# Kernel tuning notes

Measured on AMD Instinct MI355X. Metric: run time of the kernel, lower is better.

## Reference

```python
import jax, jax.numpy as jnp
import numpy as np

N_NODES = 50000
N_EDGES = 800000
IN_DIM = 128
HEADS = 4
CH = 64
NEG_SLOPE = 0.2


def _gat_conv(x, src, dst, W, a_src, a_dst, bias):
    """PyG-style GATConv (self-loops already appended to src/dst).
    x: [N, F_in], W: [F_in, H*C], a_src/a_dst: [H, C], bias: [H*C]."""
    n = x.shape[0]
    h = (x @ W).reshape(n, HEADS, CH)                      # [N, H, C]
    alpha_s = (h * a_src).sum(-1)                          # [N, H]
    alpha_d = (h * a_dst).sum(-1)                          # [N, H]
    e = jax.nn.leaky_relu(alpha_s[src] + alpha_d[dst], NEG_SLOPE)  # [E, H]
    m = jax.ops.segment_max(e, dst, num_segments=n)        # segment softmax over dst
    e = jnp.exp(e - m[dst])
    denom = jax.ops.segment_sum(e, dst, num_segments=n)
    alpha = e / (denom[dst] + 1e-16)                       # [E, H]
    out = jax.ops.segment_sum(h[src] * alpha[:, :, None], dst, num_segments=n)
    return out.reshape(n, HEADS * CH) + bias               # concat=True


def setup_inputs() -> dict:
    key = jax.random.key(0)
    ks = jax.random.split(key, 10)
    x = jax.random.normal(ks[0], (N_NODES, IN_DIM), dtype=jnp.float32)
    edge_index = jax.random.randint(ks[1], (2, N_EDGES), 0, N_NODES, dtype=jnp.int64)
    s1 = 1.0 / np.sqrt(IN_DIM)
    s2 = 1.0 / np.sqrt(HEADS * CH)
    return {
        "x": x,
        "edge_index": edge_index,
        "W1": jax.random.normal(ks[2], (IN_DIM, HEADS * CH), dtype=jnp.float32) * s1,
        "a_src1": jax.random.normal(ks[3], (HEADS, CH), dtype=jnp.float32) * s1,
        "a_dst1": jax.random.normal(ks[4], (HEADS, CH), dtype=jnp.float32) * s1,
        "b1": jnp.zeros((HEADS * CH,), dtype=jnp.float32),
        "W2": jax.random.normal(ks[5], (HEADS * CH, HEADS * CH), dtype=jnp.float32) * s2,
        "a_src2": jax.random.normal(ks[6], (HEADS, CH), dtype=jnp.float32) * s2,
        "a_dst2": jax.random.normal(ks[7], (HEADS, CH), dtype=jnp.float32) * s2,
        "b2": jnp.zeros((HEADS * CH,), dtype=jnp.float32),
        "fc_w": jax.random.normal(ks[8], (HEADS * CH, 1), dtype=jnp.float32) * s2,
        "fc_b": jnp.zeros((1,), dtype=jnp.float32),
    }


def reference(x, edge_index, W1, a_src1, a_dst1, b1, W2, a_src2, a_dst2, b2, fc_w, fc_b):
    n = x.shape[0]
    loop = jnp.arange(n, dtype=edge_index.dtype)           # PyG GATConv adds self-loops
    src = jnp.concatenate([edge_index[0], loop])
    dst = jnp.concatenate([edge_index[1], loop])
    h = jax.nn.elu(_gat_conv(x, src, dst, W1, a_src1, a_dst1, b1))
    h = jax.nn.elu(_gat_conv(h, src, dst, W2, a_src2, a_dst2, b2))
    return jax.nn.sigmoid(h @ fc_w + fc_b)                 # [N, 1]
```

## Files before the change

### kernel.cpp

```cpp
#include <hip/hip_runtime.h>
#include <hip/hip_bf16.h>

#define N_NODES 50000
#define N_EDGES 800000
#define NCHUNK 256
#define EPC 3125
#define NBUCKET 196
#define SCAN_N 50176
#define SCAN_BLOCKS 196

typedef __attribute__((ext_vector_type(8))) short bf16x8;
typedef __attribute__((ext_vector_type(4))) float f32x4;
typedef __attribute__((ext_vector_type(2))) float f32x2;
typedef unsigned short ushort_t;

__device__ __forceinline__ float bf2f(unsigned short u) {
    union { unsigned u32; float f; } v; v.u32 = (unsigned)u << 16; return v.f;
}
__device__ __forceinline__ unsigned short f2bf(float f) {
    __hip_bfloat16 h = __float2bfloat16(f);
    return *reinterpret_cast<unsigned short*>(&h);
}
__device__ __forceinline__ f32x2 bfpair(unsigned u) {
    union { unsigned a; float f; } lo, hi;
    lo.a = u << 16;
    hi.a = u & 0xFFFF0000u;
    f32x2 r; r.x = lo.f; r.y = hi.f; return r;
}
__device__ __forceinline__ void pkfma(f32x2& d, f32x2 a, f32x2 b) {
    asm("v_pk_fma_f32 %0, %1, %2, %0" : "+v"(d) : "v"(a), "v"(b));
}
__device__ __forceinline__ void gload16(const void* src, void* lds) {
    __builtin_amdgcn_global_load_lds(
        (const __attribute__((address_space(1))) unsigned int*)src,
        (__attribute__((address_space(3))) unsigned int*)lds, 16, 0, 0);
}

__device__ __forceinline__ int detect_is32_block(const unsigned* __restrict__ w,
                                                 int* s_is32, int tid) {
    if (tid == 0) {
        unsigned o = 0;
#pragma unroll
        for (int k = 1; k < 32; k += 2) o |= w[k];
        *s_is32 = (o != 0u);
    }
    __syncthreads();
    return *s_is32;
}

__device__ __forceinline__ int edge_elem(const unsigned* __restrict__ w, int is32, long long idx) {
    return is32 ? (int)w[idx] : (int)w[2 * idx];
}

#define CONV_BLOCKS 6250
#define PREP_W_BLOCKS (CONV_BLOCKS + 128 + 256)
__global__ void __launch_bounds__(256) prep_kernel(const float* __restrict__ x,
                                                   ushort_t* __restrict__ xbf,
                                                   const float* __restrict__ W1,
                                                   ushort_t* __restrict__ W1t,
                                                   const float* __restrict__ W2,
                                                   ushort_t* __restrict__ W2t,
                                                   const unsigned* __restrict__ ew,
                                                   int* __restrict__ chunkHist) {
    int b = blockIdx.x, t = threadIdx.x;
    if (b < CONV_BLOCKS) {
        int i = b * 256 + t;
        float4 v = ((const float4*)x)[i];
        ushort4 o;
        o.x = f2bf(v.x); o.y = f2bf(v.y); o.z = f2bf(v.z); o.w = f2bf(v.w);
        ((ushort4*)xbf)[i] = o;
    } else if (b < CONV_BLOCKS + 128) {
        int id = (b - CONV_BLOCKS) * 256 + t;
        int n = id >> 7, k = id & 127;
        W1t[id] = f2bf(W1[k * 256 + n]);
    } else if (b < CONV_BLOCKS + 128 + 256) {
        int id = (b - CONV_BLOCKS - 128) * 256 + t;
        int n = id >> 8, k = id & 255;
        W2t[id] = f2bf(W2[k * 256 + n]);
    } else {
        __shared__ int s_is32;
        __shared__ int hist[NBUCKET];
        int c = b - PREP_W_BLOCKS;
        int is32 = detect_is32_block(ew, &s_is32, t);
        for (int k = t; k < NBUCKET; k += 256) hist[k] = 0;
        __syncthreads();
        long long e0 = (long long)c * EPC;
        for (int k = t; k < EPC; k += 256) {
            int d = edge_elem(ew, is32, (long long)N_EDGES + e0 + k);
            atomicAdd(&hist[d >> 8], 1);
        }
        __syncthreads();
        for (int k = t; k < NBUCKET; k += 256)
            chunkHist[k * NCHUNK + c] = hist[k];
    }
}

__global__ void __launch_bounds__(256) scan1_kernel(const int* __restrict__ in,
                                                    int* __restrict__ excl, int* __restrict__ bsum) {
    __shared__ int s[256];
    int b = blockIdx.x, t = threadIdx.x, i = b * 256 + t;
    int v = in[i];
    s[t] = v;
    __syncthreads();
    for (int off = 1; off < 256; off <<= 1) {
        int y = (t >= off) ? s[t - off] : 0;
        __syncthreads();
        s[t] += y;
        __syncthreads();
    }
    excl[i] = s[t] - v;
    if (t == 255) bsum[b] = s[255];
}

__global__ void __launch_bounds__(256) scan2_kernel(const int* __restrict__ bsum,
                                                    int* __restrict__ boff) {
    __shared__ int s[256];
    int t = threadIdx.x;
    int v = (t < SCAN_BLOCKS) ? bsum[t] : 0;
    s[t] = v;
    __syncthreads();
    for (int off = 1; off < 256; off <<= 1) {
        int y = (t >= off) ? s[t - off] : 0;
        __syncthreads();
        s[t] += y;
        __syncthreads();
    }
    if (t < SCAN_BLOCKS) boff[t] = s[t] - v;
}

__global__ void __launch_bounds__(256) scan3_kernel(const int* __restrict__ boff,
                                                    int* __restrict__ excl) {
    int i = blockIdx.x * 256 + threadIdx.x;
    excl[i] += boff[blockIdx.x];
}

__global__ void __launch_bounds__(256) bucket_scatter_kernel(const unsigned* __restrict__ ew,
                                                             const int* __restrict__ chunkOff,
                                                             unsigned* __restrict__ ebuf) {
    __shared__ int s_is32;
    __shared__ int cur[NBUCKET];
    int t = threadIdx.x, b = blockIdx.x;
    int is32 = detect_is32_block(ew, &s_is32, t);
    for (int k = t; k < NBUCKET; k += 256) cur[k] = chunkOff[k * NCHUNK + b];
    __syncthreads();
    long long e0 = (long long)b * EPC;
    for (int k = t; k < EPC; k += 256) {
        long long e = e0 + k;
        unsigned s = (unsigned)edge_elem(ew, is32, e);
        int d = edge_elem(ew, is32, (long long)N_EDGES + e);
        int pos = atomicAdd(&cur[d >> 8], 1);
        ebuf[pos] = s | ((unsigned)d << 16);
    }
}

__global__ void __launch_bounds__(256) bucket_sort_kernel(const unsigned* __restrict__ ebuf,
                                                          const int* __restrict__ chunkOff,
                                                          unsigned* __restrict__ edge_csr,
                                                          int* __restrict__ row_ptr,
                                                          int* __restrict__ dhist) {
    __shared__ int cnt[256];
    __shared__ int s[256];
    __shared__ int dh[64];
    int b = blockIdx.x, t = threadIdx.x;
    int start = chunkOff[b * NCHUNK];
    int end = (b + 1 < NBUCKET) ? chunkOff[(b + 1) * NCHUNK] : N_EDGES;
    cnt[t] = 0;
    if (t < 64) dh[t] = 0;
    __syncthreads();
    for (int e = start + t; e < end; e += 256) {
        int d = (int)(ebuf[e] >> 16);
        atomicAdd(&cnt[d & 255], 1);
    }
    __syncthreads();
    int node = b * 256 + t;
    int mydeg = cnt[t];
    if (node < N_NODES) atomicAdd(&dh[mydeg < 63 ? mydeg : 63], 1);
    s[t] = mydeg;
    __syncthreads();
    for (int off = 1; off < 256; off <<= 1) {
        int y = (t >= off) ? s[t - off] : 0;
        __syncthreads();
        s[t] += y;
        __syncthreads();
    }
    int excl = s[t] - mydeg;
    if (node <= N_NODES) row_ptr[node] = start + excl;
    cnt[t] = start + excl;
    __syncthreads();
    for (int e = start + t; e < end; e += 256) {
        unsigned pk = ebuf[e];
        int pos = atomicAdd(&cnt[(pk >> 16) & 255], 1);
        edge_csr[pos] = pk;
    }
    if (t < 64 && dh[t]) atomicAdd(&dhist[t], dh[t]);
}

__global__ void __launch_bounds__(64) dscan_kernel(const int* __restrict__ dhist,
                                                   int* __restrict__ dcur) {
    int t = threadIdx.x;
    int v = dhist[t];
    int sum = v;
#pragma unroll
    for (int off = 1; off < 64; off <<= 1) {
        int y = __shfl_up(sum, off, 64);
        if (t >= off) sum += y;
    }
    dcur[t] = sum - v;
}

__global__ void __launch_bounds__(256) dscatter_kernel(const int* __restrict__ row_ptr,
                                                       int* __restrict__ dcur,
                                                       int* __restrict__ perm) {
    __shared__ int lh[64], lbase[64];
    int t = threadIdx.x, i = blockIdx.x * 256 + t;
    if (t < 64) lh[t] = 0;
    __syncthreads();
    int deg = 0;
    if (i < N_NODES) {
        deg = row_ptr[i + 1] - row_ptr[i];
        if (deg > 63) deg = 63;
        atomicAdd(&lh[deg], 1);
    }
    __syncthreads();
    if (t < 64) {
        lbase[t] = lh[t] ? atomicAdd(&dcur[t], lh[t]) : 0;
        lh[t] = 0;
    }
    __syncthreads();
    if (i < N_NODES) {
        int rank = atomicAdd(&lh[deg], 1);
        perm[lbase[deg] + rank] = i;
    }
}

template <int K>
__global__ void __launch_bounds__(256) mfma_gemm_kernel(const ushort_t* __restrict__ A,
                                                        const ushort_t* __restrict__ Wt,
                                                        void* __restrict__ Cv, int M,
                                                        const float* __restrict__ a_src,
                                                        const float* __restrict__ a_dst,
                                                        float* __restrict__ alpha_s,
                                                        float* __restrict__ alpha_d) {
    constexpr int CPR = K / 8;
    constexpr int NT = K / 64;
    __shared__ ushort_t Bs[64 * K];
    __shared__ ushort_t As[2][64 * 64];
    __shared__ float ps[64][2], pd[64][2];

    int tid = threadIdx.x;
    int wave = tid >> 6, lane = tid & 63;
    int l15 = lane & 15, l4 = lane >> 4;
    int wr = wave >> 1, wc = wave & 1;
    int colblock = blockIdx.x;
    int rowblock = blockIdx.y;

    for (int base = 0; base < 64 * CPR; base += 256) {
        int p = base + wave * 64 + lane;
        int row = p / CPR;
        int cs = p % CPR;
        int c = cs ^ (row & 7);
        const ushort_t* src = Wt + (long long)(colblock * 64 + row) * K + c * 8;
        void* dst = ((char*)Bs) + (base + wave * 64) * 16;
        gload16(src, dst);
    }
    {
        int r = lane >> 3, cs = lane & 7;
        int c = cs ^ r;
#pragma unroll
        for (int q = 0; q < 2; ++q) {
            int lrow = wave * 16 + q * 8;
            int grow = rowblock * 64 + lrow + r;
            if (grow >= M) grow = M - 1;
            const ushort_t* src = A + (long long)grow * K + c * 8;
            void* dst = ((char*)&As[0][0]) + lrow * 128;
            gload16(src, dst);
        }
    }
    __syncthreads();

    f32x4 acc[2][2] = {};
#pragma unroll
    for (int t = 0; t < NT; ++t) {
        if (t + 1 < NT) {
            int r = lane >> 3, cs = lane & 7;
            int c = cs ^ r;
#pragma unroll
            for (int q = 0; q < 2; ++q) {
                int lrow = wave * 16 + q * 8;
                int grow = rowblock * 64 + lrow + r;
                if (grow >= M) grow = M - 1;
                const ushort_t* src = A + (long long)grow * K + (t + 1) * 64 + c * 8;
                void* dst = ((char*)&As[(t + 1) & 1][0]) + lrow * 128;
                gload16(src, dst);
            }
        }
        const ushort_t* At = &As[t & 1][0];
#pragma unroll
        for (int w = 0; w < 2; ++w) {
            bf16x8 a[2], b[2];
#pragma unroll
            for (int mi = 0; mi < 2; ++mi) {
                int row = wr * 32 + mi * 16 + l15;
                int slot = (w * 4 + l4) ^ (l15 & 7);
                a[mi] = *(const bf16x8*)&At[row * 64 + slot * 8];
            }
#pragma unroll
            for (int ni = 0; ni < 2; ++ni) {
                int brow = wc * 32 + ni * 16 + l15;
                int slot = (t * 8 + w * 4 + l4) ^ (l15 & 7);
                b[ni] = *(const bf16x8*)&Bs[brow * CPR * 8 + slot * 8];
            }
#pragma unroll
            for (int mi = 0; mi < 2; ++mi)
#pragma unroll
                for (int ni = 0; ni < 2; ++ni)
                    acc[mi][ni] = __builtin_amdgcn_mfma_f32_16x16x32_bf16(a[mi], b[ni],
                                                                          acc[mi][ni], 0, 0, 0);
        }
        __syncthreads();
    }

    {
        float as0 = a_src[colblock * 64 + wc * 32 + l15];
        float as1 = a_src[colblock * 64 + wc * 32 + 16 + l15];
        float ad0 = a_dst[colblock * 64 + wc * 32 + l15];
        float ad1 = a_dst[colblock * 64 + wc * 32 + 16 + l15];
#pragma unroll
        for (int mi = 0; mi < 2; ++mi)
#pragma unroll
            for (int q = 0; q < 4; ++q) {
                float sv = acc[mi][0][q] * as0 + acc[mi][1][q] * as1;
                float dv = acc[mi][0][q] * ad0 + acc[mi][1][q] * ad1;
#pragma unroll
                for (int w = 1; w < 16; w <<= 1) {
                    sv += __shfl_xor(sv, w, 64);
                    dv += __shfl_xor(dv, w, 64);
                }
                if (l15 == 0) {
                    int row = wr * 32 + mi * 16 + l4 * 4 + q;
                    ps[row][wc] = sv;
                    pd[row][wc] = dv;
                }
            }
    }

    ushort_t* ep = ((ushort_t*)&As[0][0]) + wave * 1280;
#pragma unroll
    for (int mi = 0; mi < 2; ++mi)
#pragma unroll
        for (int ni = 0; ni < 2; ++ni)
#pragma unroll
            for (int q = 0; q < 4; ++q) {
                int row = mi * 16 + l4 * 4 + q;
                int col = ni * 16 + l15;
                ep[row * 40 + col] = f2bf(acc[mi][ni][q]);
            }
    __syncthreads();
#pragma unroll
    for (int j = 0; j < 2; ++j) {
        int p = lane * 2 + j;
        int row = p >> 2, seg = p & 3;
        uint4 v = *(const uint4*)&ep[row * 40 + seg * 8];
        int grow = rowblock * 64 + wr * 32 + row;
        int gcol = colblock * 64 + wc * 32 + seg * 8;
        if (grow < M) {
            f32x2 f01 = bfpair(v.x), f23 = bfpair(v.y);
            f32x2 f45 = bfpair(v.z), f67 = bfpair(v.w);
            int d0 = 0, d1 = 0;
            d0 = __builtin_amdgcn_cvt_pk_fp8_f32(f01.x, f01.y, d0, false);
            d0 = __builtin_amdgcn_cvt_pk_fp8_f32(f23.x, f23.y, d0, true);
            d1 = __builtin_amdgcn_cvt_pk_fp8_f32(f45.x, f45.y, d1, false);
            d1 = __builtin_amdgcn_cvt_pk_fp8_f32(f67.x, f67.y, d1, true);
            uint2 o; o.x = (unsigned)d0; o.y = (unsigned)d1;
            *(uint2*)((char*)Cv + (long long)grow * 256 + gcol) = o;
        }
    }
    if (tid < 64) {
        int ga = rowblock * 64 + tid;
        if (ga < M) {
            alpha_s[ga * 4 + colblock] = ps[tid][0] + ps[tid][1];
            alpha_d[ga * 4 + colblock] = pd[tid][0] + pd[tid][1];
        }
    }
}

template <int LAYER>
__global__ void __launch_bounds__(256) aggregate_kernel(
    const void* __restrict__ gv, const float* __restrict__ alpha_s,
    const float* __restrict__ alpha_d, const int* __restrict__ row_ptr,
    const unsigned* __restrict__ edge_csr, const int* __restrict__ perm,
    const float* __restrict__ bias, ushort_t* __restrict__ out_bf,
    const float* __restrict__ fc_w, const float* __restrict__ fc_b,
    float* __restrict__ final_out) {
    int wave = threadIdx.x >> 6;
    int lane = threadIdx.x & 63;
    int i = __builtin_amdgcn_readfirstlane(perm[blockIdx.x * 4 + wave]);
    int hd = lane >> 4;
    const char* gb = (const char*)gv;
    unsigned loff = (unsigned)(lane << 2);

    float ad = alpha_d[i * 4 + hd];
    float e0 = alpha_s[i * 4 + hd] + ad;
    e0 = e0 > 0.f ? e0 : 0.2f * e0;
    float w0 = __expf(e0);
    f32x2 wp0; wp0.x = w0; wp0.y = w0;
    f32x2 acc01 = {0.f, 0.f}, acc23 = {0.f, 0.f};
    {
        unsigned sv = *(const unsigned*)(gb + (((unsigned)i << 8) | loff));
        pkfma(acc01, wp0, __builtin_amdgcn_cvt_pk_f32_fp8(sv, false));
        pkfma(acc23, wp0, __builtin_amdgcn_cvt_pk_f32_fp8(sv, true));
    }
    float wsum = w0;

    int p = __builtin_amdgcn_readfirstlane(row_ptr[i]);
    int p1 = __builtin_amdgcn_readfirstlane(row_ptr[i + 1]);
    for (; p + 8 <= p1; p += 8) {
        int j[8]; float as[8]; unsigned hh[8];
#pragma unroll
        for (int u = 0; u < 8; ++u)
            j[u] = (int)(edge_csr[p + u] & 0xFFFFu);
#pragma unroll
        for (int u = 0; u < 8; ++u) as[u] = alpha_s[j[u] * 4 + hd];
#pragma unroll
        for (int u = 0; u < 8; ++u)
            hh[u] = *(const unsigned*)(gb + (((unsigned)j[u] << 8) | loff));
#pragma unroll
        for (int u = 0; u < 8; ++u) {
            float e = as[u] + ad;
            e = e > 0.f ? e : 0.2f * e;
            float wt = __expf(e);
            wsum += wt;
            f32x2 wp; wp.x = wt; wp.y = wt;
            pkfma(acc01, wp, __builtin_amdgcn_cvt_pk_f32_fp8(hh[u], false));
            pkfma(acc23, wp, __builtin_amdgcn_cvt_pk_f32_fp8(hh[u], true));
        }
    }
    for (; p < p1; ++p) {
        int j = (int)(edge_csr[p] & 0xFFFFu);
        float e = alpha_s[j * 4 + hd] + ad;
        e = e > 0.f ? e : 0.2f * e;
        float wt = __expf(e);
        unsigned hj = *(const unsigned*)(gb + (((unsigned)j << 8) | loff));
        wsum += wt;
        f32x2 wp; wp.x = wt; wp.y = wt;
        pkfma(acc01, wp, __builtin_amdgcn_cvt_pk_f32_fp8(hj, false));
        pkfma(acc23, wp, __builtin_amdgcn_cvt_pk_f32_fp8(hj, true));
    }
    float inv = 1.f / (wsum + 1e-16f);
    int c = lane * 4;
    float4 b4 = *(const float4*)&bias[c];
    float o0 = acc01.x * inv + b4.x;
    float o1 = acc01.y * inv + b4.y;
    float o2 = acc23.x * inv + b4.z;
    float o3 = acc23.y * inv + b4.w;
    o0 = o0 > 0.f ? o0 : __expf(o0) - 1.f;
    o1 = o1 > 0.f ? o1 : __expf(o1) - 1.f;
    o2 = o2 > 0.f ? o2 : __expf(o2) - 1.f;
    o3 = o3 > 0.f ? o3 : __expf(o3) - 1.f;
    if (LAYER == 1) {
        ushort4 o;
        o.x = f2bf(o0); o.y = f2bf(o1); o.z = f2bf(o2); o.w = f2bf(o3);
        ((ushort4*)out_bf)[(long long)i * 64 + lane] = o;
    } else {
        float4 fw = *(const float4*)&fc_w[c];
        float dot = o0 * fw.x + o1 * fw.y + o2 * fw.z + o3 * fw.w;
#pragma unroll
        for (int off = 32; off; off >>= 1) dot += __shfl_down(dot, off, 64);
        if (lane == 0) final_out[i] = 1.f / (1.f + __expf(-(dot + fc_b[0])));
    }
}

extern "C" void kernel_launch(void* const* d_in, const int* in_sizes, int n_in,
                              void* d_out, int out_size, void* d_ws, size_t ws_size,
                              hipStream_t stream) {
    const float* x   = (const float*)d_in[0];
    const unsigned* ei = (const unsigned*)d_in[1];
    const float* W1  = (const float*)d_in[2];
    const float* as1 = (const float*)d_in[3];
    const float* ad1 = (const float*)d_in[4];
    const float* b1  = (const float*)d_in[5];
    const float* W2  = (const float*)d_in[6];
    const float* as2 = (const float*)d_in[7];
    const float* ad2 = (const float*)d_in[8];
    const float* b2  = (const float*)d_in[9];
    const float* fcw = (const float*)d_in[10];
    const float* fcb = (const float*)d_in[11];

    char* ws = (char*)d_ws;
    void* g1f8         = (void*)(ws + 0);
    void* g2f8         = (void*)(ws + 12800000);
    ushort_t* hactbf   = (ushort_t*)(ws + 25600000);
    ushort_t* xbf      = (ushort_t*)(ws + 51200000);
    ushort_t* W1t      = (ushort_t*)(ws + 64000000);
    ushort_t* W2t      = (ushort_t*)(ws + 64100000);
    float* asv         = (float*)(ws + 64300000);
    float* adv         = (float*)(ws + 65100000);
    int* row_ptr       = (int*)(ws + 65900000);
    int* chunkHist     = (int*)(ws + 66110000);
    int* chunkOff      = (int*)(ws + 66320000);
    unsigned* ebuf     = (unsigned*)(ws + 66530000);
    unsigned* edge_csr = (unsigned*)(ws + 69730000);
    int* perm          = (int*)(ws + 72930000);
    int* bsum          = (int*)(ws + 73130000);
    int* boff          = (int*)(ws + 73131024);
    int* dhist         = (int*)(ws + 73132048);
    int* dcur          = (int*)(ws + 73132304);

    hipMemsetAsync(dhist, 0, 64 * 4, stream);

    prep_kernel<<<PREP_W_BLOCKS + NCHUNK, 256, 0, stream>>>(x, xbf, W1, W1t, W2, W2t,
                                                            ei, chunkHist);
    scan1_kernel<<<SCAN_BLOCKS, 256, 0, stream>>>(chunkHist, chunkOff, bsum);
    scan2_kernel<<<1, 256, 0, stream>>>(bsum, boff);
    scan3_kernel<<<SCAN_BLOCKS, 256, 0, stream>>>(boff, chunkOff);
    bucket_scatter_kernel<<<NCHUNK, 256, 0, stream>>>(ei, chunkOff, ebuf);
    bucket_sort_kernel<<<NBUCKET, 256, 0, stream>>>(ebuf, chunkOff, edge_csr, row_ptr, dhist);
    dscan_kernel<<<1, 64, 0, stream>>>(dhist, dcur);
    dscatter_kernel<<<SCAN_BLOCKS, 256, 0, stream>>>(row_ptr, dcur, perm);

    mfma_gemm_kernel<128><<<dim3(4, (N_NODES + 63) / 64), 256, 0, stream>>>(
        xbf, W1t, g1f8, N_NODES, as1, ad1, asv, adv);
    aggregate_kernel<1><<<N_NODES / 4, 256, 0, stream>>>(g1f8, asv, adv, row_ptr, edge_csr, perm,
                                                         b1, hactbf, nullptr, nullptr, nullptr);
    mfma_gemm_kernel<256><<<dim3(4, (N_NODES + 63) / 64), 256, 0, stream>>>(
        hactbf, W2t, g2f8, N_NODES, as2, ad2, asv, adv);
    aggregate_kernel<2><<<N_NODES / 4, 256, 0, stream>>>(g2f8, asv, adv, row_ptr, edge_csr, perm,
                                                         b2, nullptr, fcw, fcb, (float*)d_out);
}
```

Before: 185.9 us.

## Fuse scan and degree-scan kernels, drop memset, deepen aggregate unroll

Removes the single-block scan2 kernel by having each scan3 block sum its own prefix of block sums, and folds the dscan kernel into dscatter, where every block recomputes the 64-entry degree prefix itself. The hipMemset of dhist moves into prep_kernel, which now also zeroes dcur, so the launch count drops by three. The aggregate loop adds a 16-edge batch and a 4-edge batch ahead of the existing 8 and 1 paths to expose more memory-level parallelism on high-degree nodes, at some cost in register pressure. Zeroing dhist inside prep_kernel is safe only because bucket_sort, the first writer, runs after prep_kernel.

```diff
diff --git a/kernel.cpp b/kernel.cpp
--- a/kernel.cpp
+++ b/kernel.cpp
@@ -61,9 +61,12 @@
                                                    const float* __restrict__ W2,
                                                    ushort_t* __restrict__ W2t,
                                                    const unsigned* __restrict__ ew,
-                                                   int* __restrict__ chunkHist) {
+                                                   int* __restrict__ chunkHist,
+                                                   int* __restrict__ dhist,
+                                                   int* __restrict__ dcur) {
     int b = blockIdx.x, t = threadIdx.x;
     if (b < CONV_BLOCKS) {
+        if (b == 0 && t < 64) { dhist[t] = 0; dcur[t] = 0; }
         int i = b * 256 + t;
         float4 v = ((const float4*)x)[i];
         ushort4 o;
@@ -112,26 +115,19 @@
     if (t == 255) bsum[b] = s[255];
 }
 
-__global__ void __launch_bounds__(256) scan2_kernel(const int* __restrict__ bsum,
-                                                    int* __restrict__ boff) {
-    __shared__ int s[256];
-    int t = threadIdx.x;
-    int v = (t < SCAN_BLOCKS) ? bsum[t] : 0;
-    s[t] = v;
-    __syncthreads();
-    for (int off = 1; off < 256; off <<= 1) {
-        int y = (t >= off) ? s[t - off] : 0;
-        __syncthreads();
-        s[t] += y;
-        __syncthreads();
-    }
-    if (t < SCAN_BLOCKS) boff[t] = s[t] - v;
-}
-
-__global__ void __launch_bounds__(256) scan3_kernel(const int* __restrict__ boff,
+__global__ void __launch_bounds__(256) scan3_kernel(const int* __restrict__ bsum,
                                                     int* __restrict__ excl) {
-    int i = blockIdx.x * 256 + threadIdx.x;
-    excl[i] += boff[blockIdx.x];
+    __shared__ int sboff;
+    int b = blockIdx.x, t = threadIdx.x;
+    if (t < 64) {
+        int add = 0;
+        for (int k = t; k < b; k += 64) add += bsum[k];
+#pragma unroll
+        for (int off = 32; off; off >>= 1) add += __shfl_down(add, off, 64);
+        if (t == 0) sboff = add;
+    }
+    __syncthreads();
+    excl[b * 256 + t] += sboff;
 }
 
 __global__ void __launch_bounds__(256) bucket_scatter_kernel(const unsigned* __restrict__ ew,
@@ -195,25 +191,23 @@
     if (t < 64 && dh[t]) atomicAdd(&dhist[t], dh[t]);
 }
 
-__global__ void __launch_bounds__(64) dscan_kernel(const int* __restrict__ dhist,
-                                                   int* __restrict__ dcur) {
-    int t = threadIdx.x;
-    int v = dhist[t];
-    int sum = v;
-#pragma unroll
-    for (int off = 1; off < 64; off <<= 1) {
-        int y = __shfl_up(sum, off, 64);
-        if (t >= off) sum += y;
-    }
-    dcur[t] = sum - v;
-}
-
 __global__ void __launch_bounds__(256) dscatter_kernel(const int* __restrict__ row_ptr,
+                                                       const int* __restrict__ dhist,
                                                        int* __restrict__ dcur,
                                                        int* __restrict__ perm) {
-    __shared__ int lh[64], lbase[64];
+    __shared__ int lh[64], lbase[64], sbase[64];
     int t = threadIdx.x, i = blockIdx.x * 256 + t;
-    if (t < 64) lh[t] = 0;
+    if (t < 64) {
+        int v = dhist[t];
+        int sum = v;
+#pragma unroll
+        for (int off = 1; off < 64; off <<= 1) {
+            int y = __shfl_up(sum, off, 64);
+            if (t >= off) sum += y;
+        }
+        sbase[t] = sum - v;
+        lh[t] = 0;
+    }
     __syncthreads();
     int deg = 0;
     if (i < N_NODES) {
@@ -223,7 +217,7 @@
     }
     __syncthreads();
     if (t < 64) {
-        lbase[t] = lh[t] ? atomicAdd(&dcur[t], lh[t]) : 0;
+        lbase[t] = lh[t] ? (sbase[t] + atomicAdd(&dcur[t], lh[t])) : 0;
         lh[t] = 0;
     }
     __syncthreads();
@@ -384,6 +378,32 @@
     }
 }
 
+template <int U>
+__device__ __forceinline__ void agg_batch(int p, const unsigned* __restrict__ edge_csr,
+                                          const float* __restrict__ alpha_s,
+                                          const char* __restrict__ gb, unsigned loff,
+                                          int hd, float ad, float& wsum,
+                                          f32x2& acc01, f32x2& acc23) {
+    int j[U]; float as[U]; unsigned hh[U];
+#pragma unroll
+    for (int u = 0; u < U; ++u) j[u] = (int)(edge_csr[p + u] & 0xFFFFu);
+#pragma unroll
+    for (int u = 0; u < U; ++u) as[u] = alpha_s[j[u] * 4 + hd];
+#pragma unroll
+    for (int u = 0; u < U; ++u)
+        hh[u] = *(const unsigned*)(gb + (((unsigned)j[u] << 8) | loff));
+#pragma unroll
+    for (int u = 0; u < U; ++u) {
+        float e = as[u] + ad;
+        e = e > 0.f ? e : 0.2f * e;
+        float wt = __expf(e);
+        wsum += wt;
+        f32x2 wp; wp.x = wt; wp.y = wt;
+        pkfma(acc01, wp, __builtin_amdgcn_cvt_pk_f32_fp8(hh[u], false));
+        pkfma(acc23, wp, __builtin_amdgcn_cvt_pk_f32_fp8(hh[u], true));
+    }
+}
+
 template <int LAYER>
 __global__ void __launch_bounds__(256) aggregate_kernel(
     const void* __restrict__ gv, const float* __restrict__ alpha_s,
@@ -403,10 +423,10 @@
     float e0 = alpha_s[i * 4 + hd] + ad;
     e0 = e0 > 0.f ? e0 : 0.2f * e0;
     float w0 = __expf(e0);
-    f32x2 wp0; wp0.x = w0; wp0.y = w0;
     f32x2 acc01 = {0.f, 0.f}, acc23 = {0.f, 0.f};
     {
         unsigned sv = *(const unsigned*)(gb + (((unsigned)i << 8) | loff));
+        f32x2 wp0; wp0.x = w0; wp0.y = w0;
         pkfma(acc01, wp0, __builtin_amdgcn_cvt_pk_f32_fp8(sv, false));
         pkfma(acc23, wp0, __builtin_amdgcn_cvt_pk_f32_fp8(sv, true));
     }
@@ -414,38 +434,15 @@
 
     int p = __builtin_amdgcn_readfirstlane(row_ptr[i]);
     int p1 = __builtin_amdgcn_readfirstlane(row_ptr[i + 1]);
-    for (; p + 8 <= p1; p += 8) {
-        int j[8]; float as[8]; unsigned hh[8];
-#pragma unroll
-        for (int u = 0; u < 8; ++u)
-            j[u] = (int)(edge_csr[p + u] & 0xFFFFu);
-#pragma unroll
-        for (int u = 0; u < 8; ++u) as[u] = alpha_s[j[u] * 4 + hd];
-#pragma unroll
-        for (int u = 0; u < 8; ++u)
-            hh[u] = *(const unsigned*)(gb + (((unsigned)j[u] << 8) | loff));
-#pragma unroll
-        for (int u = 0; u < 8; ++u) {
-            float e = as[u] + ad;
-            e = e > 0.f ? e : 0.2f * e;
-            float wt = __expf(e);
-            wsum += wt;
-            f32x2 wp; wp.x = wt; wp.y = wt;
-            pkfma(acc01, wp, __builtin_amdgcn_cvt_pk_f32_fp8(hh[u], false));
-            pkfma(acc23, wp, __builtin_amdgcn_cvt_pk_f32_fp8(hh[u], true));
-        }
-    }
-    for (; p < p1; ++p) {
-        int j = (int)(edge_csr[p] & 0xFFFFu);
-        float e = alpha_s[j * 4 + hd] + ad;
-        e = e > 0.f ? e : 0.2f * e;
-        float wt = __expf(e);
-        unsigned hj = *(const unsigned*)(gb + (((unsigned)j << 8) | loff));
-        wsum += wt;
-        f32x2 wp; wp.x = wt; wp.y = wt;
-        pkfma(acc01, wp, __builtin_amdgcn_cvt_pk_f32_fp8(hj, false));
-        pkfma(acc23, wp, __builtin_amdgcn_cvt_pk_f32_fp8(hj, true));
-    }
+    for (; p + 16 <= p1; p += 16)
+        agg_batch<16>(p, edge_csr, alpha_s, gb, loff, hd, ad, wsum, acc01, acc23);
+    for (; p + 8 <= p1; p += 8)
+        agg_batch<8>(p, edge_csr, alpha_s, gb, loff, hd, ad, wsum, acc01, acc23);
+    for (; p + 4 <= p1; p += 4)
+        agg_batch<4>(p, edge_csr, alpha_s, gb, loff, hd, ad, wsum, acc01, acc23);
+    for (; p < p1; ++p)
+        agg_batch<1>(p, edge_csr, alpha_s, gb, loff, hd, ad, wsum, acc01, acc23);
+
     float inv = 1.f / (wsum + 1e-16f);
     int c = lane * 4;
     float4 b4 = *(const float4*)&bias[c];
@@ -502,21 +499,16 @@
     unsigned* edge_csr = (unsigned*)(ws + 69730000);
     int* perm          = (int*)(ws + 72930000);
     int* bsum          = (int*)(ws + 73130000);
-    int* boff          = (int*)(ws + 73131024);
     int* dhist         = (int*)(ws + 73132048);
     int* dcur          = (int*)(ws + 73132304);
 
-    hipMemsetAsync(dhist, 0, 64 * 4, stream);
-
     prep_kernel<<<PREP_W_BLOCKS + NCHUNK, 256, 0, stream>>>(x, xbf, W1, W1t, W2, W2t,
-                                                            ei, chunkHist);
+                                                            ei, chunkHist, dhist, dcur);
     scan1_kernel<<<SCAN_BLOCKS, 256, 0, stream>>>(chunkHist, chunkOff, bsum);
-    scan2_kernel<<<1, 256, 0, stream>>>(bsum, boff);
-    scan3_kernel<<<SCAN_BLOCKS, 256, 0, stream>>>(boff, chunkOff);
+    scan3_kernel<<<SCAN_BLOCKS, 256, 0, stream>>>(bsum, chunkOff);
     bucket_scatter_kernel<<<NCHUNK, 256, 0, stream>>>(ei, chunkOff, ebuf);
     bucket_sort_kernel<<<NBUCKET, 256, 0, stream>>>(ebuf, chunkOff, edge_csr, row_ptr, dhist);
-    dscan_kernel<<<1, 64, 0, stream>>>(dhist, dcur);
-    dscatter_kernel<<<SCAN_BLOCKS, 256, 0, stream>>>(row_ptr, dcur, perm);
+    dscatter_kernel<<<SCAN_BLOCKS, 256, 0, stream>>>(row_ptr, dhist, dcur, perm);
 
     mfma_gemm_kernel<128><<<dim3(4, (N_NODES + 63) / 64), 256, 0, stream>>>(
         xbf, W1t, g1f8, N_NODES, as1, ad1, asv, adv);
```

Measured after the change: 176.5 us. 1.05x faster.
